# Kernel optimization log

Measured on AMD Instinct MI355X. Metric: run time of the kernel, lower is better.

## Reference

```python
import jax, jax.numpy as jnp
import numpy as np

B, T, H, V = 32, 128, 1024, 32000


def setup_inputs() -> dict:
    key = jax.random.key(0)
    ks = jax.random.split(key, 10)
    s = 0.02
    return {
        "y_input": jax.random.normal(ks[0], (B, T), dtype=jnp.float32),
        "encoder_hidden_states": jax.random.normal(ks[1], (B, H), dtype=jnp.float32),
        "W_h": jax.random.normal(ks[2], (H, H), dtype=jnp.float32) * s,   # h_projection (no bias)
        "W_c": jax.random.normal(ks[3], (H, H), dtype=jnp.float32) * s,   # c_projection (no bias)
        "W_ih": jax.random.normal(ks[4], (4 * H, 1 + H), dtype=jnp.float32) * s,
        "W_hh": jax.random.normal(ks[5], (4 * H, H), dtype=jnp.float32) * s,
        "b_ih": jax.random.normal(ks[6], (4 * H,), dtype=jnp.float32) * s,
        "b_hh": jax.random.normal(ks[7], (4 * H,), dtype=jnp.float32) * s,
        "W_out": jax.random.normal(ks[8], (V, H), dtype=jnp.float32) * s,
        "b_out": jax.random.normal(ks[9], (V,), dtype=jnp.float32) * s,
    }


def reference(y_input, encoder_hidden_states, W_h, W_c, W_ih, W_hh, b_ih, b_hh, W_out, b_out):
    # init hidden/cell from encoder states (bias-free projections)
    h0 = encoder_hidden_states @ W_h.T  # [B, H]
    c0 = encoder_hidden_states @ W_c.T  # [B, H]

    def step(carry, x_t):
        h, c = carry
        ybar = jnp.concatenate([x_t[:, None], h], axis=-1)           # [B, 1+H]
        gates = ybar @ W_ih.T + b_ih + h @ W_hh.T + b_hh             # [B, 4H]
        i, f, g, o = jnp.split(gates, 4, axis=-1)                    # torch LSTMCell gate order
        i = jax.nn.sigmoid(i)
        f = jax.nn.sigmoid(f)
        g = jnp.tanh(g)
        o = jax.nn.sigmoid(o)
        c_new = f * c + i * g
        h_new = o * jnp.tanh(c_new)
        return (h_new, c_new), h_new

    _, hs = jax.lax.scan(step, (h0, c0), y_input.T)  # hs: [T, B, H]
    logits = hs @ W_out.T + b_out                    # [T, B, V]
    return jnp.transpose(logits, (1, 2, 0))          # [B, V, T]
```

## Files before the change

kernel.cpp:

```cpp
#include <hip/hip_runtime.h>
#include <hip/hip_bf16.h>
#include <stdint.h>

#define B_ 32
#define T_ 128
#define H_ 1024
#define V_ 32000
#define NBLK_REC 64

typedef unsigned short u16;
typedef __attribute__((ext_vector_type(8))) short short8;
typedef __attribute__((ext_vector_type(4))) float f32x4;

static __device__ __forceinline__ u16 f2bf(float f) {
    uint32_t u = __float_as_uint(f);
    uint32_t r = (u + 0x7FFFu + ((u >> 16) & 1u)) >> 16;
    return (u16)r;
}

static __device__ __forceinline__ float sigmf(float x) {
    return 1.0f / (1.0f + __expf(-x));
}

static __device__ __forceinline__ float tanh_f(float x) {
    x = fminf(fmaxf(x, -20.f), 20.f);
    float e = __expf(2.f * x);
    return (e - 1.f) / (e + 1.f);
}

static __device__ __forceinline__ void gload16(const void* g, void* l) {
    __builtin_amdgcn_global_load_lds(
        (const __attribute__((address_space(1))) uint32_t*)g,
        (__attribute__((address_space(3))) uint32_t*)(uint32_t)(uintptr_t)l,
        16, 0, 0);
}

__global__ void prep_fused(const float* __restrict__ Wih, const float* __restrict__ Whh,
                           const float* __restrict__ bih, const float* __restrict__ bhh,
                           const float* __restrict__ Wout,
                           const float* __restrict__ enc, const float* __restrict__ Wh,
                           const float* __restrict__ Wcp,
                           u16* __restrict__ Wc, float* __restrict__ wx,
                           float* __restrict__ biasc, unsigned* __restrict__ flags,
                           u16* __restrict__ Wo, u16* __restrict__ h0,
                           float* __restrict__ c0) {
    int blk = blockIdx.x;
    int tid = threadIdx.x;

    if (blk < 16384) {
        int idx = blk * 256 + tid;
        int r = idx >> 10, k = idx & 1023;
        float v = Wih[r * (H_ + 1) + 1 + k] + Whh[idx];
        Wc[idx] = f2bf(v);
        if (k == 0) {
            wx[r] = Wih[r * (H_ + 1)];
            biasc[r] = bih[r] + bhh[r];
        }
        if (idx < 2048) flags[idx] = 0u;
        return;
    }
    if (blk < 48384) {
        long long i = (long long)(blk - 16384) * 256 + tid;
        f32x4 v = *(const f32x4*)(Wout + i * 4);
        uint2 o;
        o.x = (uint32_t)f2bf(v[0]) | ((uint32_t)f2bf(v[1]) << 16);
        o.y = (uint32_t)f2bf(v[2]) | ((uint32_t)f2bf(v[3]) << 16);
        *(uint2*)(Wo + i * 4) = o;
        return;
    }
    {
        int gwid = (blk - 48384) * 4 + (tid >> 6);
        int lane = tid & 63;
        int sel = gwid >> 10;
        int j = gwid & 1023;
        const float* W = sel ? Wcp : Wh;
        const float* wrow = W + (size_t)j * H_;
        f32x4 wv[4];
#pragma unroll
        for (int it = 0; it < 4; ++it)
            wv[it] = *(const f32x4*)(wrow + it * 256 + lane * 4);
#pragma unroll 2
        for (int b = 0; b < B_; ++b) {
            const float* erow = enc + (size_t)b * H_;
            float acc = 0.f;
#pragma unroll
            for (int it = 0; it < 4; ++it) {
                f32x4 ev = *(const f32x4*)(erow + it * 256 + lane * 4);
                acc += wv[it][0] * ev[0] + wv[it][1] * ev[1] + wv[it][2] * ev[2] + wv[it][3] * ev[3];
            }
#pragma unroll
            for (int s = 32; s >= 1; s >>= 1) acc += __shfl_xor(acc, s, 64);
            if (lane == 0) {
                if (sel) c0[(size_t)b * H_ + j] = acc;
                else     h0[(size_t)b * H_ + j] = f2bf(acc);
            }
        }
    }
}

__global__ __launch_bounds__(512, 2) void fused_all(
    const u16* __restrict__ Wc, const float* __restrict__ wx,
    const float* __restrict__ biasc, const u16* __restrict__ h0,
    const float* __restrict__ c0, const float* __restrict__ y,
    u16* __restrict__ A, unsigned* __restrict__ flags,
    const u16* __restrict__ Wo, const float* __restrict__ bout,
    float* __restrict__ out) {
    __shared__ __align__(16) u16 sb[65536];

    int tid = threadIdx.x;
    int lane = tid & 63;

    if (blockIdx.x < NBLK_REC) {
        __builtin_amdgcn_s_setprio(2);
        float* red = (float*)sb;
        float* cs  = red + 8 * 2112;
        float* wxs = cs + 16 * 33;
        float* bcs = wxs + 64;
        float* ys  = bcs + 64;

        int kw = tid >> 6;
        int bid = blockIdx.x;
        int j0 = bid * 16;
        int jl = lane & 15;
        int kc = (lane >> 4) * 8;
        int jlx = tid & 15, pb = tid >> 4;

        short8 afr[4][4];
        {
            const u16* abase = Wc + (size_t)(j0 + jl) * H_ + kw * 128 + kc;
#pragma unroll
            for (int g = 0; g < 4; ++g)
#pragma unroll
                for (int ks = 0; ks < 4; ++ks)
                    afr[g][ks] = *(const short8*)(abase + (size_t)g * H_ * H_ + ks * 32);
        }
#pragma unroll
        for (int g = 0; g < 4; ++g)
#pragma unroll
            for (int ks = 0; ks < 4; ++ks)
                asm volatile("" : "+v"(afr[g][ks]));

        if (tid < 64) {
            int g = tid >> 4, qq = tid & 15;
            wxs[tid] = wx[(size_t)g * H_ + j0 + qq];
            bcs[tid] = biasc[(size_t)g * H_ + j0 + qq];
        }
#pragma unroll
        for (int i = tid; i < B_ * T_; i += 512)
            ys[(i >> 7) * 129 + (i & 127)] = y[i];
        cs[jlx * 33 + pb] = c0[(size_t)pb * H_ + j0 + jlx];
        __syncthreads();

        for (int t = 0; t < T_; ++t) {
            const u16* hp = (t == 0) ? h0 : (A + (size_t)(t - 1) * B_ * H_);

            if (t > 0) {
                const unsigned* fp = &flags[(kw * 8 + (lane & 7)) * 32];
                unsigned target = (unsigned)t;
                int guard = 0;
                for (;;) {
                    unsigned v = __hip_atomic_load(fp, __ATOMIC_RELAXED, __HIP_MEMORY_SCOPE_AGENT);
                    if (__all(v >= target)) break;
                    if (++guard > 20000000) break;
                }
                __atomic_signal_fence(__ATOMIC_ACQUIRE);
            }

            short8 bf0[4], bf1[4];
            {
                const u16* hb = hp + (size_t)jl * H_ + kw * 128 + kc;
#pragma unroll
                for (int ks = 0; ks < 4; ++ks) {
                    bf0[ks] = *(const short8*)(hb + ks * 32);
                    bf1[ks] = *(const short8*)(hb + (size_t)16 * H_ + ks * 32);
                }
            }
            f32x4 acc[4][2] = {};
#pragma unroll
            for (int ks = 0; ks < 4; ++ks) {
#pragma unroll
                for (int g = 0; g < 4; ++g) {
                    acc[g][0] = __builtin_amdgcn_mfma_f32_16x16x32_bf16(afr[g][ks], bf0[ks], acc[g][0], 0, 0, 0);
                    acc[g][1] = __builtin_amdgcn_mfma_f32_16x16x32_bf16(afr[g][ks], bf1[ks], acc[g][1], 0, 0, 0);
                }
            }
            int r0 = (lane >> 4) * 4;
#pragma unroll
            for (int g = 0; g < 4; ++g)
#pragma unroll
                for (int bt = 0; bt < 2; ++bt)
#pragma unroll
                    for (int r = 0; r < 4; ++r)
                        red[kw * 2112 + (g * 16 + r0 + r) * 33 + bt * 16 + jl] = acc[g][bt][r];
            __syncthreads();

            {
                float yv = ys[pb * 129 + t];
                float pg[4];
#pragma unroll
                for (int g = 0; g < 4; ++g) {
                    int row = (g * 16 + jlx) * 33 + pb;
                    float sum = red[row];
#pragma unroll
                    for (int ww = 1; ww < 8; ++ww) sum += red[ww * 2112 + row];
                    pg[g] = sum + wxs[g * 16 + jlx] * yv + bcs[g * 16 + jlx];
                }
                float iv = sigmf(pg[0]);
                float fv = sigmf(pg[1]);
                float gv = tanh_f(pg[2]);
                float ov = sigmf(pg[3]);
                float cv = fv * cs[jlx * 33 + pb] + iv * gv;
                cs[jlx * 33 + pb] = cv;
                float hv = ov * tanh_f(cv);

                unsigned h16 = (unsigned)f2bf(hv);
                unsigned oth = (unsigned)__shfl((int)h16, lane + 1, 64);
                if (!(jlx & 1)) {
                    uint32_t pk = h16 | (oth << 16);
                    __hip_atomic_store((uint32_t*)(A + ((size_t)t * B_ + pb) * H_ + j0 + jlx),
                                       pk, __ATOMIC_RELAXED, __HIP_MEMORY_SCOPE_AGENT);
                }
            }
            __syncthreads();
            if (tid == 0)
                __hip_atomic_store(&flags[bid * 32], (unsigned)(t + 1),
                                   __ATOMIC_RELAXED, __HIP_MEMORY_SCOPE_AGENT);
        }
        return;
    }

    int orig = blockIdx.x - NBLK_REC;
    int tb = orig / 500;
    int wp = orig - tb * 500;
    int xcd = wp & 7, rest = wp >> 3;
    int wg = (xcd < 4 ? xcd * 63 : 252 + (xcd - 4) * 62) + rest;
    int bb = wg / 125;
    int nb = wg - bb * 125;
    int n0g = nb << 8;

    int wid = tid >> 6;
    int wm = wid >> 2, wn = wid & 3;
    int jl = lane & 15, kq = lane >> 4;

    f32x4 acc[8][4] = {};

    auto stage = [&](int tile, int h) {
        u16* dst = sb + ((tile & 1) << 15) + (h << 13) + tid * 8;
#pragma unroll
        for (int ld = 0; ld < 2; ++ld) {
            int p = tid + (ld << 9);
            int row = p >> 3;
            int c16 = (p & 7) ^ (row & 7);
            const u16* src;
            if (h < 2)
                src = A + ((size_t)(tb * 32 + (row & 31)) * B_
                           + (size_t)(bb * 8 + h * 4 + (row >> 5))) * H_
                        + tile * 64 + c16 * 8;
            else
                src = Wo + (size_t)(n0g + ((h - 2) << 7) + row) * H_
                         + tile * 64 + c16 * 8;
            gload16(src, dst + (ld << 12));
        }
    };

    stage(0, 2); stage(0, 3);

    if (wid == 0) {
        unsigned target = (unsigned)((tb + 1) * 32);
        const unsigned* fp = &flags[lane * 32];
        int guard = 0;
        for (;;) {
            unsigned v = __hip_atomic_load(fp, __ATOMIC_RELAXED, __HIP_MEMORY_SCOPE_AGENT);
            if (__all(v >= target)) break;
            __builtin_amdgcn_s_sleep(32);
            if (++guard > 20000000) break;
        }
        __atomic_signal_fence(__ATOMIC_ACQUIRE);
    }
    __builtin_amdgcn_s_barrier();

    stage(0, 0); stage(0, 1); stage(1, 0); stage(1, 2);
    asm volatile("s_waitcnt vmcnt(4)" ::: "memory");
    __builtin_amdgcn_s_barrier();

    const int NT = 16;
    for (int tile = 0; tile < NT; ++tile) {
        const u16* buf = sb + ((tile & 1) << 15);
#pragma unroll
        for (int q = 0; q < 4; ++q) {
            const int mh = q >> 1, nh = q & 1;
            short8 af[4][2], bfr[2][2];
            const u16* bufA = buf + (mh << 13);
            const u16* bufB = buf + (1 << 14) + (nh << 13);
#pragma unroll
            for (int i = 0; i < 4; ++i) {
                int row = wm * 64 + (i << 4) + jl;
                int rx = (row & 7) << 3;
#pragma unroll
                for (int k2 = 0; k2 < 2; ++k2)
                    af[i][k2] = *(const short8*)(bufA + row * 64 + (((k2 << 5) + (kq << 3)) ^ rx));
            }
#pragma unroll
            for (int i = 0; i < 2; ++i) {
                int row = wn * 32 + (i << 4) + jl;
                int rx = (row & 7) << 3;
#pragma unroll
                for (int k2 = 0; k2 < 2; ++k2)
                    bfr[i][k2] = *(const short8*)(bufB + row * 64 + (((k2 << 5) + (kq << 3)) ^ rx));
            }
            if (q == 0) { if (tile + 1 < NT) stage(tile + 1, 1); }
            if (q == 1) { if (tile + 1 < NT) stage(tile + 1, 3); }
            if (q == 2) { if (tile + 2 < NT) stage(tile + 2, 0); }
            if (q == 3) { if (tile + 2 < NT) stage(tile + 2, 2); }

            asm volatile("" ::: "memory");
            __builtin_amdgcn_s_barrier();
            asm volatile("" ::: "memory");
            __builtin_amdgcn_s_setprio(1);
#pragma unroll
            for (int i = 0; i < 4; ++i)
#pragma unroll
                for (int jn = 0; jn < 2; ++jn)
#pragma unroll
                    for (int k2 = 0; k2 < 2; ++k2)
                        acc[mh * 4 + i][nh * 2 + jn] =
                            __builtin_amdgcn_mfma_f32_16x16x32_bf16(
                                af[i][k2], bfr[jn][k2], acc[mh * 4 + i][nh * 2 + jn], 0, 0, 0);
            __builtin_amdgcn_s_setprio(0);
            if (q == 3) {
                if (tile < 14) asm volatile("s_waitcnt vmcnt(4)" ::: "memory");
                else           asm volatile("s_waitcnt vmcnt(0)" ::: "memory");
            }
            asm volatile("" ::: "memory");
            __builtin_amdgcn_s_barrier();
        }
    }

#pragma unroll
    for (int nt = 0; nt < 4; ++nt) {
        int n = n0g + ((nt >> 1) << 7) + wn * 32 + ((nt & 1) << 4) + jl;
        float bias = bout[n];
#pragma unroll
        for (int mt = 0; mt < 8; ++mt) {
            int mh = mt >> 2, i = mt & 3;
            int bo = bb * 8 + mh * 4 + wm * 2 + (i >> 1);
            f32x4 v = acc[mt][nt];
            v[0] += bias; v[1] += bias; v[2] += bias; v[3] += bias;
            float* dst = out + ((size_t)bo * V_ + n) * T_ + tb * 32 + ((i & 1) << 4) + (kq << 2);
            *(f32x4*)dst = v;
        }
    }
}

extern "C" void kernel_launch(void* const* d_in, const int* in_sizes, int n_in,
                              void* d_out, int out_size, void* d_ws, size_t ws_size,
                              hipStream_t stream) {
    const float* y    = (const float*)d_in[0];
    const float* enc  = (const float*)d_in[1];
    const float* Wh   = (const float*)d_in[2];
    const float* Wcp  = (const float*)d_in[3];
    const float* Wih  = (const float*)d_in[4];
    const float* Whh  = (const float*)d_in[5];
    const float* bih  = (const float*)d_in[6];
    const float* bhh  = (const float*)d_in[7];
    const float* Wout = (const float*)d_in[8];
    const float* bout = (const float*)d_in[9];

    uint8_t* ws = (uint8_t*)d_ws;
    u16*  Wcomb = (u16*)ws;
    u16*  Wo    = (u16*)(ws + 8388608);
    float* wx    = (float*)(ws + 8388608 + 65536000);
    float* biasc = wx + 4096;
    u16*  h0    = (u16*)(biasc + 4096);
    float* c     = (float*)(h0 + 32 * 1024);
    u16*  A     = (u16*)(c + 32 * 1024);
    unsigned* flags = (unsigned*)(A + (size_t)4096 * 1024);

    prep_fused<<<48896, 256, 0, stream>>>(Wih, Whh, bih, bhh, Wout, enc, Wh, Wcp,
                                          Wcomb, wx, biasc, flags, Wo, h0, c);

    fused_all<<<NBLK_REC + 2000, 512, 0, stream>>>(
        Wcomb, wx, biasc, h0, c, y, A, flags, Wo, bout, (float*)d_out);
}
```

Before: 732.0 us.

## Replace per-step flag barrier with sentinel-polled hidden-state mirror buffer

The per-step flag spin-wait between recurrent blocks is replaced by polling the previous step's hidden state directly. A mirror buffer is prefilled with 0xFFFFFFFF sentinels and read with cache-bypassing loads until no sentinel remains. The reduction buffer in LDS is double-buffered so one barrier per step can be dropped. Flags are now only bumped every 32 steps for the output-GEMM consumers. This adds extra global writes and sentinel-fill work, drops occupancy to 1 block per CU, and relies on an all-ones bf16 pair never being a valid value.

```diff
diff --git a/kernel.cpp b/kernel.cpp
--- a/kernel.cpp
+++ b/kernel.cpp
@@ -11,6 +11,7 @@
 typedef unsigned short u16;
 typedef __attribute__((ext_vector_type(8))) short short8;
 typedef __attribute__((ext_vector_type(4))) float f32x4;
+typedef __attribute__((ext_vector_type(4))) unsigned u32x4;
 
 static __device__ __forceinline__ u16 f2bf(float f) {
     uint32_t u = __float_as_uint(f);
@@ -33,6 +34,12 @@
         (const __attribute__((address_space(1))) uint32_t*)g,
         (__attribute__((address_space(3))) uint32_t*)(uint32_t)(uintptr_t)l,
         16, 0, 0);
+}
+
+static __device__ __forceinline__ u32x4 cload16(const void* p) {
+    u32x4 r;
+    asm volatile("global_load_dwordx4 %0, %1, off sc0 sc1" : "=v"(r) : "v"(p));
+    return r;
 }
 
 __global__ void prep_fused(const float* __restrict__ Wih, const float* __restrict__ Whh,
@@ -43,7 +50,7 @@
                            u16* __restrict__ Wc, float* __restrict__ wx,
                            float* __restrict__ biasc, unsigned* __restrict__ flags,
                            u16* __restrict__ Wo, u16* __restrict__ h0,
-                           float* __restrict__ c0) {
+                           float* __restrict__ c0, unsigned* __restrict__ Amir32) {
     int blk = blockIdx.x;
     int tid = threadIdx.x;
 
@@ -57,6 +64,7 @@
             biasc[r] = bih[r] + bhh[r];
         }
         if (idx < 2048) flags[idx] = 0u;
+        if (idx < 2097152) Amir32[idx] = 0xFFFFFFFFu;
         return;
     }
     if (blk < 48384) {
@@ -98,14 +106,14 @@
     }
 }
 
-__global__ __launch_bounds__(512, 2) void fused_all(
+__global__ __launch_bounds__(512, 1) void fused_all(
     const u16* __restrict__ Wc, const float* __restrict__ wx,
     const float* __restrict__ biasc, const u16* __restrict__ h0,
     const float* __restrict__ c0, const float* __restrict__ y,
     u16* __restrict__ A, unsigned* __restrict__ flags,
     const u16* __restrict__ Wo, const float* __restrict__ bout,
-    float* __restrict__ out) {
-    __shared__ __align__(16) u16 sb[65536];
+    float* __restrict__ out, u16* __restrict__ Amir) {
+    __shared__ __align__(16) u16 sb[77184];
 
     int tid = threadIdx.x;
     int lane = tid & 63;
@@ -113,7 +121,7 @@
     if (blockIdx.x < NBLK_REC) {
         __builtin_amdgcn_s_setprio(2);
         float* red = (float*)sb;
-        float* cs  = red + 8 * 2112;
+        float* cs  = red + 2 * 8 * 2112;
         float* wxs = cs + 16 * 33;
         float* bcs = wxs + 64;
         float* ys  = bcs + 64;
@@ -152,29 +160,42 @@
         __syncthreads();
 
         for (int t = 0; t < T_; ++t) {
-            const u16* hp = (t == 0) ? h0 : (A + (size_t)(t - 1) * B_ * H_);
-
-            if (t > 0) {
-                const unsigned* fp = &flags[(kw * 8 + (lane & 7)) * 32];
-                unsigned target = (unsigned)t;
-                int guard = 0;
-                for (;;) {
-                    unsigned v = __hip_atomic_load(fp, __ATOMIC_RELAXED, __HIP_MEMORY_SCOPE_AGENT);
-                    if (__all(v >= target)) break;
-                    if (++guard > 20000000) break;
-                }
-                __atomic_signal_fence(__ATOMIC_ACQUIRE);
-            }
-
             short8 bf0[4], bf1[4];
-            {
-                const u16* hb = hp + (size_t)jl * H_ + kw * 128 + kc;
+            if (t == 0) {
+                const u16* hb = h0 + (size_t)jl * H_ + kw * 128 + kc;
 #pragma unroll
                 for (int ks = 0; ks < 4; ++ks) {
                     bf0[ks] = *(const short8*)(hb + ks * 32);
                     bf1[ks] = *(const short8*)(hb + (size_t)16 * H_ + ks * 32);
                 }
-            }
+            } else {
+                const u16* hb = Amir + ((size_t)(t - 1) * B_ + jl) * H_ + kw * 128 + kc;
+                u32x4 q0[4], q1[4];
+                int guard = 0;
+                for (;;) {
+#pragma unroll
+                    for (int ks = 0; ks < 4; ++ks) {
+                        q0[ks] = cload16(hb + ks * 32);
+                        q1[ks] = cload16(hb + (size_t)16 * H_ + ks * 32);
+                    }
+                    asm volatile("s_waitcnt vmcnt(0)" ::: "memory");
+                    __builtin_amdgcn_sched_barrier(0);
+                    unsigned bad = 0;
+#pragma unroll
+                    for (int ks = 0; ks < 4; ++ks)
+#pragma unroll
+                        for (int d = 0; d < 4; ++d)
+                            bad |= (unsigned)(q0[ks][d] == 0xFFFFFFFFu) |
+                                   (unsigned)(q1[ks][d] == 0xFFFFFFFFu);
+                    if (!__any(bad) || ++guard > 50000) break;
+                }
+#pragma unroll
+                for (int ks = 0; ks < 4; ++ks) {
+                    bf0[ks] = __builtin_bit_cast(short8, q0[ks]);
+                    bf1[ks] = __builtin_bit_cast(short8, q1[ks]);
+                }
+            }
+
             f32x4 acc[4][2] = {};
 #pragma unroll
             for (int ks = 0; ks < 4; ++ks) {
@@ -184,6 +205,7 @@
                     acc[g][1] = __builtin_amdgcn_mfma_f32_16x16x32_bf16(afr[g][ks], bf1[ks], acc[g][1], 0, 0, 0);
                 }
             }
+            float* redp = red + (t & 1) * 16896;
             int r0 = (lane >> 4) * 4;
 #pragma unroll
             for (int g = 0; g < 4; ++g)
@@ -191,8 +213,9 @@
                 for (int bt = 0; bt < 2; ++bt)
 #pragma unroll
                     for (int r = 0; r < 4; ++r)
-                        red[kw * 2112 + (g * 16 + r0 + r) * 33 + bt * 16 + jl] = acc[g][bt][r];
-            __syncthreads();
+                        redp[kw * 2112 + (g * 16 + r0 + r) * 33 + bt * 16 + jl] = acc[g][bt][r];
+            asm volatile("s_waitcnt lgkmcnt(0)" ::: "memory");
+            __builtin_amdgcn_s_barrier();
 
             {
                 float yv = ys[pb * 129 + t];
@@ -200,9 +223,9 @@
 #pragma unroll
                 for (int g = 0; g < 4; ++g) {
                     int row = (g * 16 + jlx) * 33 + pb;
-                    float sum = red[row];
-#pragma unroll
-                    for (int ww = 1; ww < 8; ++ww) sum += red[ww * 2112 + row];
+                    float sum = redp[row];
+#pragma unroll
+                    for (int ww = 1; ww < 8; ++ww) sum += redp[ww * 2112 + row];
                     pg[g] = sum + wxs[g * 16 + jlx] * yv + bcs[g * 16 + jlx];
                 }
                 float iv = sigmf(pg[0]);
@@ -217,14 +240,19 @@
                 unsigned oth = (unsigned)__shfl((int)h16, lane + 1, 64);
                 if (!(jlx & 1)) {
                     uint32_t pk = h16 | (oth << 16);
-                    __hip_atomic_store((uint32_t*)(A + ((size_t)t * B_ + pb) * H_ + j0 + jlx),
-                                       pk, __ATOMIC_RELAXED, __HIP_MEMORY_SCOPE_AGENT);
-                }
-            }
-            __syncthreads();
-            if (tid == 0)
-                __hip_atomic_store(&flags[bid * 32], (unsigned)(t + 1),
-                                   __ATOMIC_RELAXED, __HIP_MEMORY_SCOPE_AGENT);
+                    size_t off = ((size_t)t * B_ + pb) * H_ + j0 + jlx;
+                    __hip_atomic_store((uint32_t*)(A + off), pk,
+                                       __ATOMIC_RELAXED, __HIP_MEMORY_SCOPE_AGENT);
+                    __hip_atomic_store((uint32_t*)(Amir + off), pk,
+                                       __ATOMIC_RELAXED, __HIP_MEMORY_SCOPE_AGENT);
+                }
+            }
+            if (((t + 1) & 31) == 0) {
+                asm volatile("s_waitcnt vmcnt(0)" ::: "memory");
+                if (lane == 0)
+                    __hip_atomic_fetch_add(&flags[bid * 32], 1u,
+                                           __ATOMIC_RELAXED, __HIP_MEMORY_SCOPE_AGENT);
+            }
         }
         return;
     }
@@ -266,7 +294,7 @@
     stage(0, 2); stage(0, 3);
 
     if (wid == 0) {
-        unsigned target = (unsigned)((tb + 1) * 32);
+        unsigned target = 8u * (unsigned)(tb + 1);
         const unsigned* fp = &flags[lane * 32];
         int guard = 0;
         for (;;) {
@@ -375,10 +403,12 @@
     float* c     = (float*)(h0 + 32 * 1024);
     u16*  A     = (u16*)(c + 32 * 1024);
     unsigned* flags = (unsigned*)(A + (size_t)4096 * 1024);
+    u16*  Amir  = (u16*)(flags + 2048);
 
     prep_fused<<<48896, 256, 0, stream>>>(Wih, Whh, bih, bhh, Wout, enc, Wh, Wcp,
-                                          Wcomb, wx, biasc, flags, Wo, h0, c);
+                                          Wcomb, wx, biasc, flags, Wo, h0, c,
+                                          (unsigned*)Amir);
 
     fused_all<<<NBLK_REC + 2000, 512, 0, stream>>>(
-        Wcomb, wx, biasc, h0, c, y, A, flags, Wo, bout, (float*)d_out);
-}
+        Wcomb, wx, biasc, h0, c, y, A, flags, Wo, bout, (float*)d_out, Amir);
+}
```

New measurement: 1.042 ms. 1.42x slower.

## Fold weight prep and initial-state projection into the persistent fused kernel

Applied to the files above, without the earlier changes.

Removes the separate prep kernel. Recurrent blocks now build their bf16 combined gate weights directly from Wih+Whh, and compute h0/c0 from the encoder states inside the kernel. h0 is written to slot 0 of A, which shifts all timestep indices by one. The first 128 output-projection blocks convert W_out to bf16 and announce completion through new flags; every projection block waits on those flags before staging tiles. This overlaps the weight conversion with the recurrence, but it adds per-block initial work on the serial recurrent path and a new cross-block dependency.

```diff
diff --git a/kernel.cpp b/kernel.cpp
--- a/kernel.cpp
+++ b/kernel.cpp
@@ -35,75 +35,19 @@
         16, 0, 0);
 }
 
-__global__ void prep_fused(const float* __restrict__ Wih, const float* __restrict__ Whh,
-                           const float* __restrict__ bih, const float* __restrict__ bhh,
-                           const float* __restrict__ Wout,
-                           const float* __restrict__ enc, const float* __restrict__ Wh,
-                           const float* __restrict__ Wcp,
-                           u16* __restrict__ Wc, float* __restrict__ wx,
-                           float* __restrict__ biasc, unsigned* __restrict__ flags,
-                           u16* __restrict__ Wo, u16* __restrict__ h0,
-                           float* __restrict__ c0) {
-    int blk = blockIdx.x;
-    int tid = threadIdx.x;
-
-    if (blk < 16384) {
-        int idx = blk * 256 + tid;
-        int r = idx >> 10, k = idx & 1023;
-        float v = Wih[r * (H_ + 1) + 1 + k] + Whh[idx];
-        Wc[idx] = f2bf(v);
-        if (k == 0) {
-            wx[r] = Wih[r * (H_ + 1)];
-            biasc[r] = bih[r] + bhh[r];
-        }
-        if (idx < 2048) flags[idx] = 0u;
-        return;
-    }
-    if (blk < 48384) {
-        long long i = (long long)(blk - 16384) * 256 + tid;
-        f32x4 v = *(const f32x4*)(Wout + i * 4);
-        uint2 o;
-        o.x = (uint32_t)f2bf(v[0]) | ((uint32_t)f2bf(v[1]) << 16);
-        o.y = (uint32_t)f2bf(v[2]) | ((uint32_t)f2bf(v[3]) << 16);
-        *(uint2*)(Wo + i * 4) = o;
-        return;
-    }
-    {
-        int gwid = (blk - 48384) * 4 + (tid >> 6);
-        int lane = tid & 63;
-        int sel = gwid >> 10;
-        int j = gwid & 1023;
-        const float* W = sel ? Wcp : Wh;
-        const float* wrow = W + (size_t)j * H_;
-        f32x4 wv[4];
-#pragma unroll
-        for (int it = 0; it < 4; ++it)
-            wv[it] = *(const f32x4*)(wrow + it * 256 + lane * 4);
-#pragma unroll 2
-        for (int b = 0; b < B_; ++b) {
-            const float* erow = enc + (size_t)b * H_;
-            float acc = 0.f;
-#pragma unroll
-            for (int it = 0; it < 4; ++it) {
-                f32x4 ev = *(const f32x4*)(erow + it * 256 + lane * 4);
-                acc += wv[it][0] * ev[0] + wv[it][1] * ev[1] + wv[it][2] * ev[2] + wv[it][3] * ev[3];
-            }
-#pragma unroll
-            for (int s = 32; s >= 1; s >>= 1) acc += __shfl_xor(acc, s, 64);
-            if (lane == 0) {
-                if (sel) c0[(size_t)b * H_ + j] = acc;
-                else     h0[(size_t)b * H_ + j] = f2bf(acc);
-            }
-        }
-    }
+__global__ void zero_flags(unsigned* __restrict__ flags) {
+    int idx = blockIdx.x * 256 + threadIdx.x;
+    flags[idx] = 0u;
 }
 
 __global__ __launch_bounds__(512, 2) void fused_all(
-    const u16* __restrict__ Wc, const float* __restrict__ wx,
-    const float* __restrict__ biasc, const u16* __restrict__ h0,
-    const float* __restrict__ c0, const float* __restrict__ y,
+    const float* __restrict__ Wih, const float* __restrict__ Whh,
+    const float* __restrict__ bih, const float* __restrict__ bhh,
+    const float* __restrict__ enc, const float* __restrict__ Wh,
+    const float* __restrict__ Wcp, const float* __restrict__ Wout,
+    const float* __restrict__ y,
     u16* __restrict__ A, unsigned* __restrict__ flags,
-    const u16* __restrict__ Wo, const float* __restrict__ bout,
+    u16* __restrict__ Wo, const float* __restrict__ bout,
     float* __restrict__ out) {
     __shared__ __align__(16) u16 sb[65536];
 
@@ -126,14 +70,19 @@
         int jlx = tid & 15, pb = tid >> 4;
 
         short8 afr[4][4];
-        {
-            const u16* abase = Wc + (size_t)(j0 + jl) * H_ + kw * 128 + kc;
-#pragma unroll
-            for (int g = 0; g < 4; ++g)
-#pragma unroll
-                for (int ks = 0; ks < 4; ++ks)
-                    afr[g][ks] = *(const short8*)(abase + (size_t)g * H_ * H_ + ks * 32);
-        }
+#pragma unroll
+        for (int g = 0; g < 4; ++g)
+#pragma unroll
+            for (int ks = 0; ks < 4; ++ks) {
+                int row = g * H_ + j0 + jl;
+                const float* pih = Wih + (size_t)row * (H_ + 1) + 1 + kw * 128 + kc + ks * 32;
+                const float* phh = Whh + (size_t)row * H_ + kw * 128 + kc + ks * 32;
+                short8 s;
+#pragma unroll
+                for (int e = 0; e < 8; ++e)
+                    s[e] = (short)f2bf(pih[e] + phh[e]);
+                afr[g][ks] = s;
+            }
 #pragma unroll
         for (int g = 0; g < 4; ++g)
 #pragma unroll
@@ -141,22 +90,44 @@
                 asm volatile("" : "+v"(afr[g][ks]));
 
         if (tid < 64) {
-            int g = tid >> 4, qq = tid & 15;
-            wxs[tid] = wx[(size_t)g * H_ + j0 + qq];
-            bcs[tid] = biasc[(size_t)g * H_ + j0 + qq];
+            int row = (tid >> 4) * H_ + j0 + (tid & 15);
+            wxs[tid] = Wih[(size_t)row * (H_ + 1)];
+            bcs[tid] = bih[row] + bhh[row];
         }
 #pragma unroll
         for (int i = tid; i < B_ * T_; i += 512)
             ys[(i >> 7) * 129 + (i & 127)] = y[i];
-        cs[jlx * 33 + pb] = c0[(size_t)pb * H_ + j0 + jlx];
+
+        {
+            const float* er  = enc + (size_t)pb * H_;
+            const float* whr = Wh  + (size_t)(j0 + jlx) * H_;
+            const float* wcr = Wcp + (size_t)(j0 + jlx) * H_;
+            f32x4 ah = {0.f, 0.f, 0.f, 0.f}, ac = {0.f, 0.f, 0.f, 0.f};
+#pragma unroll 4
+            for (int k4 = 0; k4 < H_ / 4; ++k4) {
+                f32x4 ev = *(const f32x4*)(er + k4 * 4);
+                ah += ev * (*(const f32x4*)(whr + k4 * 4));
+                ac += ev * (*(const f32x4*)(wcr + k4 * 4));
+            }
+            cs[jlx * 33 + pb] = ac[0] + ac[1] + ac[2] + ac[3];
+            float h0v = ah[0] + ah[1] + ah[2] + ah[3];
+            unsigned h16 = (unsigned)f2bf(h0v);
+            unsigned oth = (unsigned)__shfl((int)h16, lane + 1, 64);
+            if (!(jlx & 1)) {
+                uint32_t pk = h16 | (oth << 16);
+                __hip_atomic_store((uint32_t*)(A + (size_t)pb * H_ + j0 + jlx),
+                                   pk, __ATOMIC_RELAXED, __HIP_MEMORY_SCOPE_AGENT);
+            }
+        }
         __syncthreads();
+        if (tid == 0)
+            __hip_atomic_store(&flags[bid * 32], 1u,
+                               __ATOMIC_RELAXED, __HIP_MEMORY_SCOPE_AGENT);
 
         for (int t = 0; t < T_; ++t) {
-            const u16* hp = (t == 0) ? h0 : (A + (size_t)(t - 1) * B_ * H_);
-
-            if (t > 0) {
+            {
                 const unsigned* fp = &flags[(kw * 8 + (lane & 7)) * 32];
-                unsigned target = (unsigned)t;
+                unsigned target = (unsigned)(t + 1);
                 int guard = 0;
                 for (;;) {
                     unsigned v = __hip_atomic_load(fp, __ATOMIC_RELAXED, __HIP_MEMORY_SCOPE_AGENT);
@@ -168,7 +139,7 @@
 
             short8 bf0[4], bf1[4];
             {
-                const u16* hb = hp + (size_t)jl * H_ + kw * 128 + kc;
+                const u16* hb = A + ((size_t)t * B_ + jl) * H_ + kw * 128 + kc;
 #pragma unroll
                 for (int ks = 0; ks < 4; ++ks) {
                     bf0[ks] = *(const short8*)(hb + ks * 32);
@@ -217,13 +188,13 @@
                 unsigned oth = (unsigned)__shfl((int)h16, lane + 1, 64);
                 if (!(jlx & 1)) {
                     uint32_t pk = h16 | (oth << 16);
-                    __hip_atomic_store((uint32_t*)(A + ((size_t)t * B_ + pb) * H_ + j0 + jlx),
+                    __hip_atomic_store((uint32_t*)(A + ((size_t)(t + 1) * B_ + pb) * H_ + j0 + jlx),
                                        pk, __ATOMIC_RELAXED, __HIP_MEMORY_SCOPE_AGENT);
                 }
             }
             __syncthreads();
             if (tid == 0)
-                __hip_atomic_store(&flags[bid * 32], (unsigned)(t + 1),
+                __hip_atomic_store(&flags[bid * 32], (unsigned)(t + 2),
                                    __ATOMIC_RELAXED, __HIP_MEMORY_SCOPE_AGENT);
         }
         return;
@@ -242,6 +213,38 @@
     int wm = wid >> 2, wn = wid & 3;
     int jl = lane & 15, kq = lane >> 4;
 
+    if (orig < 128) {
+        const int QP = 250 * H_ / 4;
+        long long qbase = (long long)orig * QP;
+        for (int i = tid; i < QP; i += 512) {
+            long long q = qbase + i;
+            f32x4 v = *(const f32x4*)(Wout + q * 4);
+            unsigned long long pk =
+                (unsigned long long)((uint32_t)f2bf(v[0]) | ((uint32_t)f2bf(v[1]) << 16)) |
+                ((unsigned long long)((uint32_t)f2bf(v[2]) | ((uint32_t)f2bf(v[3]) << 16)) << 32);
+            __hip_atomic_store((unsigned long long*)Wo + q, pk,
+                               __ATOMIC_RELAXED, __HIP_MEMORY_SCOPE_AGENT);
+        }
+        asm volatile("s_waitcnt vmcnt(0)" ::: "memory");
+        __syncthreads();
+        if (tid == 0)
+            __hip_atomic_fetch_add(&flags[2048 + (orig & 63) * 32], 1u,
+                                   __ATOMIC_RELAXED, __HIP_MEMORY_SCOPE_AGENT);
+    }
+
+    if (wid == 0) {
+        const unsigned* fp = &flags[2048 + lane * 32];
+        int guard = 0;
+        for (;;) {
+            unsigned v = __hip_atomic_load(fp, __ATOMIC_RELAXED, __HIP_MEMORY_SCOPE_AGENT);
+            if (__all(v >= 2u)) break;
+            __builtin_amdgcn_s_sleep(16);
+            if (++guard > 20000000) break;
+        }
+        __atomic_signal_fence(__ATOMIC_ACQUIRE);
+    }
+    __builtin_amdgcn_s_barrier();
+
     f32x4 acc[8][4] = {};
 
     auto stage = [&](int tile, int h) {
@@ -253,7 +256,7 @@
             int c16 = (p & 7) ^ (row & 7);
             const u16* src;
             if (h < 2)
-                src = A + ((size_t)(tb * 32 + (row & 31)) * B_
+                src = A + ((size_t)(tb * 32 + (row & 31) + 1) * B_
                            + (size_t)(bb * 8 + h * 4 + (row >> 5))) * H_
                         + tile * 64 + c16 * 8;
             else
@@ -266,7 +269,7 @@
     stage(0, 2); stage(0, 3);
 
     if (wid == 0) {
-        unsigned target = (unsigned)((tb + 1) * 32);
+        unsigned target = (unsigned)(tb * 32 + 33);
         const unsigned* fp = &flags[lane * 32];
         int guard = 0;
         for (;;) {
@@ -367,18 +370,13 @@
     const float* bout = (const float*)d_in[9];
 
     uint8_t* ws = (uint8_t*)d_ws;
-    u16*  Wcomb = (u16*)ws;
-    u16*  Wo    = (u16*)(ws + 8388608);
-    float* wx    = (float*)(ws + 8388608 + 65536000);
-    float* biasc = wx + 4096;
-    u16*  h0    = (u16*)(biasc + 4096);
-    float* c     = (float*)(h0 + 32 * 1024);
-    u16*  A     = (u16*)(c + 32 * 1024);
-    unsigned* flags = (unsigned*)(A + (size_t)4096 * 1024);
-
-    prep_fused<<<48896, 256, 0, stream>>>(Wih, Whh, bih, bhh, Wout, enc, Wh, Wcp,
-                                          Wcomb, wx, biasc, flags, Wo, h0, c);
+    u16*  Wo    = (u16*)ws;
+    u16*  A     = (u16*)(ws + 65536000);
+    unsigned* flags = (unsigned*)(ws + 65536000 + 8454144);
+
+    zero_flags<<<16, 256, 0, stream>>>(flags);
 
     fused_all<<<NBLK_REC + 2000, 512, 0, stream>>>(
-        Wcomb, wx, biasc, h0, c, y, A, flags, Wo, bout, (float*)d_out);
-}
+        Wih, Whh, bih, bhh, enc, Wh, Wcp, Wout, y,
+        A, flags, Wo, bout, (float*)d_out);
+}
```

After: 780.4 us. +6.6%, slower.

## Move W_out bf16 conversion into projection blocks to overlap with recurrence

Applied to the files above, without the earlier changes.

The fp32-to-bf16 conversion of W_out moves out of the prep kernel and into the first 128 projection blocks of the fused kernel. Those blocks convert W_out while the recurrent blocks are already running, so the conversion time can hide under the sequential LSTM steps. Each block signals completion through per-slot counters, and every projection block spins until all 64 counters reach 2 before starting its GEMM. This removes a serial prep phase but adds spin-wait overhead, and it depends on the converter blocks being resident alongside the recurrence blocks, which risks a deadlock that only the guard counter breaks.

```diff
diff --git a/kernel.cpp b/kernel.cpp
--- a/kernel.cpp
+++ b/kernel.cpp
@@ -35,15 +35,13 @@
         16, 0, 0);
 }
 
-__global__ void prep_fused(const float* __restrict__ Wih, const float* __restrict__ Whh,
-                           const float* __restrict__ bih, const float* __restrict__ bhh,
-                           const float* __restrict__ Wout,
-                           const float* __restrict__ enc, const float* __restrict__ Wh,
-                           const float* __restrict__ Wcp,
-                           u16* __restrict__ Wc, float* __restrict__ wx,
-                           float* __restrict__ biasc, unsigned* __restrict__ flags,
-                           u16* __restrict__ Wo, u16* __restrict__ h0,
-                           float* __restrict__ c0) {
+__global__ void prep_mid(const float* __restrict__ Wih, const float* __restrict__ Whh,
+                         const float* __restrict__ bih, const float* __restrict__ bhh,
+                         const float* __restrict__ enc, const float* __restrict__ Wh,
+                         const float* __restrict__ Wcp,
+                         u16* __restrict__ Wc, float* __restrict__ wx,
+                         float* __restrict__ biasc, unsigned* __restrict__ flags,
+                         u16* __restrict__ h0, float* __restrict__ c0) {
     int blk = blockIdx.x;
     int tid = threadIdx.x;
 
@@ -56,20 +54,11 @@
             wx[r] = Wih[r * (H_ + 1)];
             biasc[r] = bih[r] + bhh[r];
         }
-        if (idx < 2048) flags[idx] = 0u;
+        if (idx < 4096) flags[idx] = 0u;
         return;
     }
-    if (blk < 48384) {
-        long long i = (long long)(blk - 16384) * 256 + tid;
-        f32x4 v = *(const f32x4*)(Wout + i * 4);
-        uint2 o;
-        o.x = (uint32_t)f2bf(v[0]) | ((uint32_t)f2bf(v[1]) << 16);
-        o.y = (uint32_t)f2bf(v[2]) | ((uint32_t)f2bf(v[3]) << 16);
-        *(uint2*)(Wo + i * 4) = o;
-        return;
-    }
     {
-        int gwid = (blk - 48384) * 4 + (tid >> 6);
+        int gwid = (blk - 16384) * 4 + (tid >> 6);
         int lane = tid & 63;
         int sel = gwid >> 10;
         int j = gwid & 1023;
@@ -103,8 +92,8 @@
     const float* __restrict__ biasc, const u16* __restrict__ h0,
     const float* __restrict__ c0, const float* __restrict__ y,
     u16* __restrict__ A, unsigned* __restrict__ flags,
-    const u16* __restrict__ Wo, const float* __restrict__ bout,
-    float* __restrict__ out) {
+    u16* __restrict__ Wo, const float* __restrict__ Wout,
+    const float* __restrict__ bout, float* __restrict__ out) {
     __shared__ __align__(16) u16 sb[65536];
 
     int tid = threadIdx.x;
@@ -241,6 +230,38 @@
     int wid = tid >> 6;
     int wm = wid >> 2, wn = wid & 3;
     int jl = lane & 15, kq = lane >> 4;
+
+    if (orig < 128) {
+        const int QP = 250 * H_ / 4;
+        long long qbase = (long long)orig * QP;
+        for (int i = tid; i < QP; i += 512) {
+            long long q = qbase + i;
+            f32x4 v = *(const f32x4*)(Wout + q * 4);
+            unsigned long long pk =
+                (unsigned long long)((uint32_t)f2bf(v[0]) | ((uint32_t)f2bf(v[1]) << 16)) |
+                ((unsigned long long)((uint32_t)f2bf(v[2]) | ((uint32_t)f2bf(v[3]) << 16)) << 32);
+            __hip_atomic_store((unsigned long long*)Wo + q, pk,
+                               __ATOMIC_RELAXED, __HIP_MEMORY_SCOPE_AGENT);
+        }
+        asm volatile("s_waitcnt vmcnt(0)" ::: "memory");
+        __syncthreads();
+        if (tid == 0)
+            __hip_atomic_fetch_add(&flags[2048 + (orig & 63) * 32], 1u,
+                                   __ATOMIC_RELAXED, __HIP_MEMORY_SCOPE_AGENT);
+    }
+
+    if (wid == 0) {
+        const unsigned* fp = &flags[2048 + lane * 32];
+        int guard = 0;
+        for (;;) {
+            unsigned v = __hip_atomic_load(fp, __ATOMIC_RELAXED, __HIP_MEMORY_SCOPE_AGENT);
+            if (__all(v >= 2u)) break;
+            __builtin_amdgcn_s_sleep(16);
+            if (++guard > 20000000) break;
+        }
+        __atomic_signal_fence(__ATOMIC_ACQUIRE);
+    }
+    __builtin_amdgcn_s_barrier();
 
     f32x4 acc[8][4] = {};
 
@@ -376,9 +397,9 @@
     u16*  A     = (u16*)(c + 32 * 1024);
     unsigned* flags = (unsigned*)(A + (size_t)4096 * 1024);
 
-    prep_fused<<<48896, 256, 0, stream>>>(Wih, Whh, bih, bhh, Wout, enc, Wh, Wcp,
-                                          Wcomb, wx, biasc, flags, Wo, h0, c);
+    prep_mid<<<16896, 256, 0, stream>>>(Wih, Whh, bih, bhh, enc, Wh, Wcp,
+                                        Wcomb, wx, biasc, flags, h0, c);
 
     fused_all<<<NBLK_REC + 2000, 512, 0, stream>>>(
-        Wcomb, wx, biasc, h0, c, y, A, flags, Wo, bout, (float*)d_out);
-}
+        Wcomb, wx, biasc, h0, c, y, A, flags, Wo, Wout, bout, (float*)d_out);
+}
```

Result: faster. 690.9 us (-5.6%).
